# Kernel optimization log

Hardware: AMD Instinct MI355X
Metric: run time of the kernel (lower is better)

The kernel has to match this reference:

```python
import jax, jax.numpy as jnp
import numpy as np

# Block(type='a'): dim=256, mlp_ratio=2, qk_dim=64, att_cr=0.5 (pdim=128), sr=2, inp_group=1
DIM, QK, PD, HID, SR = 256, 64, 128, 512, 2
EPS = 1e-5
SCALE = QK ** -0.5


def _conv(x, w, stride=1, pad=0, groups=1):
    return jax.lax.conv_general_dilated(
        x, w, (stride, stride), [(pad, pad), (pad, pad)],
        feature_group_count=groups,
        dimension_numbers=('NCHW', 'OIHW', 'NCHW'))


def _bn(x, s, b):
    # BatchNorm2d in inference/reparam form: per-channel affine
    return x * s[:, None, None] + b[:, None, None]


def setup_inputs() -> dict:
    key = jax.random.key(0)
    ks = jax.random.split(key, 16)
    B, H, W = 16, 64, 64
    x = jax.random.normal(ks[0], (B, DIM, H, W), jnp.float32)
    def w(k, shape):  # conv weights
        return jax.random.normal(k, shape, jnp.float32) * 0.02
    def sb(k, c):     # bn scale / bias
        k1, k2 = jax.random.split(k)
        return (1.0 + 0.1 * jax.random.normal(k1, (c,), jnp.float32),
                0.1 * jax.random.normal(k2, (c,), jnp.float32))
    s_in, b_in = sb(ks[2], 2 * QK + DIM)
    s_k, b_k = sb(ks[4], QK)
    s_v, b_v = sb(ks[6], PD)
    s_out, b_out = sb(ks[8], DIM)
    s1, b1 = sb(ks[10], HID)
    s2, b2 = sb(ks[12], DIM)
    return dict(
        x=x,
        gn_w=1.0 + 0.1 * jax.random.normal(ks[13], (DIM,), jnp.float32),
        gn_b=0.1 * jax.random.normal(ks[14], (DIM,), jnp.float32),
        w_in=w(ks[1], (2 * QK + DIM, DIM, 3, 3)), s_in=s_in, b_in=b_in,
        w_k=w(ks[3], (QK, 1, SR, SR)), s_k=s_k, b_k=b_k,
        w_v=w(ks[5], (PD, 1, SR, SR)), s_v=s_v, b_v=b_v,
        w_out=w(ks[7], (DIM, DIM, 1, 1)), s_out=s_out, b_out=b_out,
        w1=w(ks[9], (HID, DIM, 1, 1)), s1=s1, b1=b1,
        w2=w(ks[11], (DIM, HID, 1, 1)), s2=s2, b2=b2,
    )


def reference(x, gn_w, gn_b, w_in, s_in, b_in, w_k, s_k, b_k, w_v, s_v, b_v,
              w_out, s_out, b_out, w1, s1, b1, w2, s2, b2):
    B, _, H, W = x.shape
    # --- LRSHA branch ---
    # GroupNorm(1, dim): normalize over (C,H,W) per sample, per-channel affine
    mu = jnp.mean(x, axis=(1, 2, 3), keepdims=True)
    var = jnp.var(x, axis=(1, 2, 3), keepdims=True)
    xn = (x - mu) * jax.lax.rsqrt(var + EPS)
    xn = xn * gn_w[:, None, None] + gn_b[:, None, None]
    t = _bn(_conv(xn, w_in, stride=1, pad=1), s_in, b_in)  # [B, 2*QK+DIM, H, W]
    q, k, v, u = jnp.split(t, [QK, 2 * QK, 2 * QK + PD], axis=1)
    k = _bn(_conv(k, w_k, stride=SR, groups=QK), s_k, b_k)  # [B,QK,H/2,W/2]
    v = _bn(_conv(v, w_v, stride=SR, groups=PD), s_v, b_v)  # [B,PD,H/2,W/2]
    qf = q.reshape(B, QK, H * W)          # [B, QK, N]
    kf = k.reshape(B, QK, -1)             # [B, QK, M]
    vf = v.reshape(B, PD, -1)             # [B, PD, M]
    attn = jax.nn.softmax(jnp.einsum('bcn,bcm->bnm', qf, kf) * SCALE, axis=-1)
    a = jnp.einsum('bpm,bnm->bpn', vf, attn).reshape(B, PD, H, W)
    cat = jnp.concatenate([a, u], axis=1)  # [B, DIM, H, W]
    att_out = _bn(_conv(jax.nn.relu(cat), w_out), s_out, b_out)
    x1 = x + att_out  # residual
    # --- FFN branch (1x1 conv -> ReLU -> 1x1 conv) ---
    h = jax.nn.relu(_bn(_conv(x1, w1), s1, b1))
    ffn = _bn(_conv(h, w2), s2, b2)
    return x1 + ffn
```

## Files before the change

kernel.cpp:

```cpp
#include <hip/hip_runtime.h>
#include <hip/hip_bf16.h>

#define DIM 256
#define QK 64
#define PD 128
#define HID 512
#define NPX 4096
#define NB 16
#define SCALE 0.125f
#define GN_EPS 1e-5f

typedef short bf16x8 __attribute__((ext_vector_type(8)));
typedef float f32x4 __attribute__((ext_vector_type(4)));
#define MFMA16(a, b, c) __builtin_amdgcn_mfma_f32_16x16x32_bf16(a, b, c, 0, 0, 0)

__device__ __forceinline__ unsigned f2b(float f) {
    unsigned u = __float_as_uint(f);
    return (u + 0x7fffu + ((u >> 16) & 1u)) >> 16;
}
__device__ __forceinline__ float b2f(unsigned short s) {
    return __uint_as_float((unsigned)s << 16);
}

__global__ __launch_bounds__(256) void gn_part_kernel(const float* __restrict__ x, float* __restrict__ part) {
    int chunk = blockIdx.x, b = blockIdx.y;
    const float* xp = x + (size_t)b * (DIM * NPX) + (size_t)chunk * 16384;
    float s = 0.f, ss = 0.f;
    for (int i = threadIdx.x; i < 16384; i += 256) { float v = xp[i]; s += v; ss += v * v; }
    for (int off = 32; off > 0; off >>= 1) { s += __shfl_down(s, off); ss += __shfl_down(ss, off); }
    __shared__ float red[8];
    int w = threadIdx.x >> 6;
    if ((threadIdx.x & 63) == 0) { red[w * 2] = s; red[w * 2 + 1] = ss; }
    __syncthreads();
    if (threadIdx.x == 0) {
        float S = red[0] + red[2] + red[4] + red[6];
        float SS = red[1] + red[3] + red[5] + red[7];
        part[(b * 64 + chunk) * 2] = S;
        part[(b * 64 + chunk) * 2 + 1] = SS;
    }
}

__global__ __launch_bounds__(256) void gn_final_kernel(const float* __restrict__ part,
                                                       const float* __restrict__ gn_w, const float* __restrict__ gn_b,
                                                       float* __restrict__ Aarr, float* __restrict__ Barr) {
    int b = blockIdx.x;
    float s = 0.f, ss = 0.f;
    if (threadIdx.x < 64) {
        s = part[(b * 64 + threadIdx.x) * 2];
        ss = part[(b * 64 + threadIdx.x) * 2 + 1];
        for (int off = 32; off > 0; off >>= 1) { s += __shfl_down(s, off); ss += __shfl_down(ss, off); }
    }
    __shared__ float sh[2];
    if (threadIdx.x == 0) {
        const float invN = 1.f / (float)(DIM * NPX);
        float mu = s * invN;
        float var = ss * invN - mu * mu;
        sh[0] = mu; sh[1] = rsqrtf(var + GN_EPS);
    }
    __syncthreads();
    float mu = sh[0], rstd = sh[1];
    int c = threadIdx.x;
    float g = gn_w[c] * rstd;
    Aarr[b * 256 + c] = g;
    Barr[b * 256 + c] = gn_b[c] - mu * g;
}

__global__ __launch_bounds__(256) void xnb_kernel(const float* __restrict__ x,
                                                  const float* __restrict__ Aarr, const float* __restrict__ Barr,
                                                  unsigned short* __restrict__ xb) {
    int y = blockIdx.x, b = blockIdx.y;
    int tid = threadIdx.x;
    __shared__ unsigned short tile[64 * 264];
    const float* xr = x + ((size_t)b << 20) + (size_t)y * 64;
    const float* Ab = Aarr + b * 256;
    const float* Bb = Barr + b * 256;
    for (int it = 0; it < 64; it++) {
        int lin = it * 256 + tid;
        int c = lin >> 6, px = lin & 63;
        float v = fmaf(xr[((size_t)c << 12) + px], Ab[c], Bb[c]);
        tile[px * 264 + c] = (unsigned short)f2b(v);
    }
    __syncthreads();
    unsigned short* ob = xb + (((size_t)(b * 64 + y)) << 14);
    for (int it = 0; it < 8; it++) {
        int lin = it * 256 + tid;
        int px = lin >> 5, g = lin & 31;
        *(uint4*)&ob[px * 256 + g * 8] = *(const uint4*)&tile[px * 264 + g * 8];
    }
}

__global__ __launch_bounds__(256) void wcvt_kernel(const float* __restrict__ w_in, const float* __restrict__ w_out,
                                                   const float* __restrict__ w1, const float* __restrict__ w2,
                                                   unsigned short* __restrict__ wb2, unsigned short* __restrict__ wob,
                                                   unsigned short* __restrict__ w1b, unsigned short* __restrict__ w2b) {
    int idx = blockIdx.x * 256 + threadIdx.x;
    if (idx < 884736) {
        int ci = idx & 31;
        int oc = (idx >> 5) % 384;
        int tapck = idx / 12288;
        int ck = tapck / 9, tap = tapck % 9;
        wb2[idx] = (unsigned short)f2b(w_in[((size_t)oc * 256 + ck * 32 + ci) * 9 + tap]);
    } else if (idx < 950272) {
        int j = idx - 884736;
        wob[j] = (unsigned short)f2b(w_out[j]);
    } else if (idx < 1081344) {
        int j = idx - 950272;
        w1b[j] = (unsigned short)f2b(w1[j]);
    } else if (idx < 1212416) {
        int j = idx - 1081344;
        w2b[j] = (unsigned short)f2b(w2[j]);
    }
}

__global__ __launch_bounds__(256, 3) void conv3_mfma_kernel(const unsigned short* __restrict__ xb,
                                                            const unsigned short* __restrict__ wb2,
                                                            const float* __restrict__ s_in, const float* __restrict__ b_in,
                                                            unsigned short* __restrict__ tcl) {
    int wgid = blockIdx.x;
    int tile = (wgid & 7) * 96 + (wgid >> 3);
    int ocb = tile % 6;
    int tmp = tile / 6;
    int rg2 = tmp & 7, b = tmp >> 3;
    int tid = threadIdx.x;
    int w = tid >> 6, lane = tid & 63, g = lane >> 4, l15 = lane & 15;
    __shared__ unsigned short xs[6 * 66 * 40];
    int oc0 = ocb * 64;
    if (tid < 48) {
        int row = tid >> 3, cp = (tid >> 2) & 1, gg = tid & 3;
        int col = cp ? 65 : 0;
        *(uint4*)&xs[(row * 66 + col) * 40 + gg * 8] = make_uint4(0, 0, 0, 0);
    }
    const unsigned short* xg = xb + ((size_t)b << 20);
    for (int half = 0; half < 2; half++) {
        int y0 = rg2 * 8 + half * 4;
        f32x4 acc[4][4];
#pragma unroll
        for (int o = 0; o < 4; o++)
#pragma unroll
            for (int p = 0; p < 4; p++)
#pragma unroll
                for (int r = 0; r < 4; r++) acc[o][p][r] = 0.f;
        for (int ck = 0; ck < 8; ck++) {
            int ci0 = ck * 32;
            __syncthreads();
#pragma unroll
            for (int it = 0; it < 6; it++) {
                int lin = it * 256 + tid;
                int gg = lin & 3, col = (lin >> 2) & 63, row = lin >> 8;
                int y = y0 - 1 + row;
                uint4 val = make_uint4(0, 0, 0, 0);
                if (y >= 0 && y < 64)
                    val = *(const uint4*)(xg + (((size_t)(y * 64 + col)) << 8) + ci0 + gg * 8);
                *(uint4*)&xs[(row * 66 + col + 1) * 40 + gg * 8] = val;
            }
            __syncthreads();
            const unsigned short* wp = wb2 + (size_t)ck * 9 * 384 * 32;
#pragma unroll
            for (int tap = 0; tap < 9; tap++) {
                int dy = tap / 3, dx = tap % 3;
                bf16x8 Af[4], Bf[4];
#pragma unroll
                for (int o = 0; o < 4; o++)
                    Af[o] = *(const bf16x8*)(wp + ((size_t)tap * 384 + oc0 + o * 16 + l15) * 32 + g * 8);
#pragma unroll
                for (int p = 0; p < 4; p++)
                    Bf[p] = *(const bf16x8*)&xs[((w + dy) * 66 + p * 16 + l15 + dx) * 40 + g * 8];
#pragma unroll
                for (int o = 0; o < 4; o++)
#pragma unroll
                    for (int p = 0; p < 4; p++)
                        acc[o][p] = MFMA16(Af[o], Bf[p], acc[o][p]);
            }
        }
        int y = y0 + w;
        unsigned short* tout = tcl + ((size_t)(b * 4096 + y * 64)) * 384;
#pragma unroll
        for (int o = 0; o < 4; o++) {
            int ocb4 = oc0 + o * 16 + 4 * g;
            float s0 = s_in[ocb4], s1 = s_in[ocb4 + 1], s2 = s_in[ocb4 + 2], s3 = s_in[ocb4 + 3];
            float b0 = b_in[ocb4], b1 = b_in[ocb4 + 1], b2 = b_in[ocb4 + 2], b3 = b_in[ocb4 + 3];
#pragma unroll
            for (int p = 0; p < 4; p++) {
                ushort4 h;
                h.x = (unsigned short)f2b(fmaf(acc[o][p][0], s0, b0));
                h.y = (unsigned short)f2b(fmaf(acc[o][p][1], s1, b1));
                h.z = (unsigned short)f2b(fmaf(acc[o][p][2], s2, b2));
                h.w = (unsigned short)f2b(fmaf(acc[o][p][3], s3, b3));
                *(ushort4*)&tout[(size_t)(p * 16 + l15) * 384 + ocb4] = h;
            }
        }
    }
}

__global__ __launch_bounds__(256) void dw_kernel(const unsigned short* __restrict__ tcl,
                                                 const float* __restrict__ w_k, const float* __restrict__ s_k, const float* __restrict__ b_k,
                                                 const float* __restrict__ w_v, const float* __restrict__ s_v, const float* __restrict__ b_v,
                                                 unsigned short* __restrict__ kd_t, unsigned short* __restrict__ vd_b) {
    int mg = blockIdx.x, b = blockIdx.y;
    int m0 = mg * 64;
    int tid = threadIdx.x;
    __shared__ unsigned short vt[128 * 68];
    {
        int c = tid & 63;
        float4 wk4 = *(const float4*)(w_k + c * 4);
        float sc = s_k[c], bi = b_k[c];
#pragma unroll 4
        for (int it = 0; it < 16; it++) {
            int ml = it * 4 + (tid >> 6);
            int m = m0 + ml, yo = m >> 5, xo = m & 31;
            const unsigned short* s = tcl + ((size_t)(b * 4096 + yo * 128 + xo * 2)) * 384 + 64 + c;
            float v = wk4.x * b2f(s[0]) + wk4.y * b2f(s[384]) + wk4.z * b2f(s[24576]) + wk4.w * b2f(s[24960]);
            kd_t[((size_t)(b * 1024 + m) << 6) + c] = (unsigned short)f2b(fmaf(v, sc, bi));
        }
    }
    {
        int c2 = tid & 127;
        float4 wv4 = *(const float4*)(w_v + c2 * 4);
        float sc = s_v[c2], bi = b_v[c2];
#pragma unroll 4
        for (int it = 0; it < 32; it++) {
            int ml = it * 2 + (tid >> 7);
            int m = m0 + ml, yo = m >> 5, xo = m & 31;
            const unsigned short* s = tcl + ((size_t)(b * 4096 + yo * 128 + xo * 2)) * 384 + 128 + c2;
            float v = wv4.x * b2f(s[0]) + wv4.y * b2f(s[384]) + wv4.z * b2f(s[24576]) + wv4.w * b2f(s[24960]);
            vt[c2 * 68 + ml] = (unsigned short)f2b(fmaf(v, sc, bi));
        }
    }
    __syncthreads();
    {
        int c2 = tid >> 1, part = tid & 1;
        unsigned short* dst = vd_b + (((size_t)(b * 128 + c2)) << 10) + m0 + part * 32;
        const unsigned short* src = &vt[c2 * 68 + part * 32];
#pragma unroll
        for (int j = 0; j < 8; j++)
            *(ushort4*)(dst + j * 4) = *(const ushort4*)(src + j * 4);
    }
}

__global__ __launch_bounds__(256) void attn_mfma_kernel(const unsigned short* __restrict__ tcl,
                                                        const unsigned short* __restrict__ kd_t,
                                                        const unsigned short* __restrict__ vd_b,
                                                        unsigned short* __restrict__ apx) {
    int tid = threadIdx.x;
    int wid = tid >> 6, lane = tid & 63;
    int g = lane >> 4, l15 = lane & 15;
    int b = blockIdx.y;
    int n0 = (blockIdx.x * 4 + wid) * 32;

    __shared__ char KsB[8192];
    __shared__ char VsB[16384];
    __shared__ unsigned short ot[4][32][136];

    bf16x8 qf[2][2];
#pragma unroll
    for (int nf = 0; nf < 2; nf++)
#pragma unroll
        for (int kc = 0; kc < 2; kc++)
            qf[nf][kc] = *(const bf16x8*)(tcl + ((size_t)(b * 4096 + n0 + 16 * nf + l15)) * 384 + kc * 32 + g * 8);

    f32x4 O[8][2];
#pragma unroll
    for (int pt = 0; pt < 8; pt++)
#pragma unroll
        for (int nf = 0; nf < 2; nf++)
#pragma unroll
            for (int r = 0; r < 4; r++) O[pt][nf][r] = 0.f;
    float mr[2] = {-1e30f, -1e30f}, lr[2] = {0.f, 0.f};

    const unsigned short* kb = kd_t + ((size_t)b << 16);
    const unsigned short* vb = vd_b + ((size_t)(b * 128) << 10);

    union BU { unsigned u[4]; bf16x8 v; };
    int srcA = l15 + ((g & 1) << 5);
    int srcB = srcA + 16;
    bool hi = (g >> 1) != 0;
    int srow = tid >> 3, sch = tid & 7;

    for (int mt = 0; mt < 16; mt++) {
        int m0 = mt * 64;
        __syncthreads();
#pragma unroll
        for (int it = 0; it < 2; it++) {
            int row = it * 32 + srow;
            uint4 v = *(const uint4*)(kb + (((size_t)(m0 + row)) << 6) + sch * 8);
            *(uint4*)(KsB + row * 128 + ((sch * 16) ^ ((row & 7) << 4))) = v;
        }
#pragma unroll
        for (int it = 0; it < 4; it++) {
            int row = it * 32 + srow;
            uint4 v = *(const uint4*)(vb + (((size_t)row) << 10) + m0 + sch * 8);
            *(uint4*)(VsB + row * 128 + ((sch * 16) ^ ((row & 7) << 4))) = v;
        }
        __syncthreads();
        f32x4 sp[4][2];
#pragma unroll
        for (int f = 0; f < 4; f++)
#pragma unroll
            for (int nf = 0; nf < 2; nf++)
#pragma unroll
                for (int r = 0; r < 4; r++) sp[f][nf][r] = 0.f;
#pragma unroll
        for (int f = 0; f < 4; f++) {
#pragma unroll
            for (int kc = 0; kc < 2; kc++) {
                bf16x8 kf = *(const bf16x8*)(KsB + (16 * f + l15) * 128 + ((kc * 64 + g * 16) ^ ((l15 & 7) << 4)));
                sp[f][0] = MFMA16(kf, qf[0][kc], sp[f][0]);
                sp[f][1] = MFMA16(kf, qf[1][kc], sp[f][1]);
            }
        }
        BU Bp[2][2];
#pragma unroll
        for (int nf = 0; nf < 2; nf++) {
            float tmax = -1e30f;
#pragma unroll
            for (int f = 0; f < 4; f++)
#pragma unroll
                for (int r = 0; r < 4; r++) tmax = fmaxf(tmax, sp[f][nf][r]);
            tmax = fmaxf(tmax, __shfl_xor(tmax, 16));
            tmax = fmaxf(tmax, __shfl_xor(tmax, 32));
            float newm = fmaxf(mr[nf], tmax * SCALE);
            float fac = __expf(mr[nf] - newm);
            float ps = 0.f;
            unsigned pl[4], ph[4];
#pragma unroll
            for (int f = 0; f < 4; f++) {
                float p0 = __expf(fmaf(sp[f][nf][0], SCALE, -newm));
                float p1 = __expf(fmaf(sp[f][nf][1], SCALE, -newm));
                float p2 = __expf(fmaf(sp[f][nf][2], SCALE, -newm));
                float p3 = __expf(fmaf(sp[f][nf][3], SCALE, -newm));
                ps += (p0 + p1) + (p2 + p3);
                pl[f] = f2b(p0) | (f2b(p1) << 16);
                ph[f] = f2b(p2) | (f2b(p3) << 16);
            }
            ps += __shfl_xor(ps, 16);
            ps += __shfl_xor(ps, 32);
            lr[nf] = fmaf(lr[nf], fac, ps);
            mr[nf] = newm;
#pragma unroll
            for (int pt = 0; pt < 8; pt++)
#pragma unroll
                for (int r = 0; r < 4; r++) O[pt][nf][r] *= fac;
#pragma unroll
            for (int kc = 0; kc < 2; kc++) {
                unsigned a0 = (unsigned)__shfl((int)pl[2 * kc], srcA);
                unsigned a1 = (unsigned)__shfl((int)ph[2 * kc], srcA);
                unsigned b0 = (unsigned)__shfl((int)pl[2 * kc + 1], srcA);
                unsigned b1 = (unsigned)__shfl((int)ph[2 * kc + 1], srcA);
                unsigned a2 = (unsigned)__shfl((int)pl[2 * kc], srcB);
                unsigned a3 = (unsigned)__shfl((int)ph[2 * kc], srcB);
                unsigned b2 = (unsigned)__shfl((int)pl[2 * kc + 1], srcB);
                unsigned b3 = (unsigned)__shfl((int)ph[2 * kc + 1], srcB);
                Bp[nf][kc].u[0] = hi ? b0 : a0;
                Bp[nf][kc].u[1] = hi ? b1 : a1;
                Bp[nf][kc].u[2] = hi ? b2 : a2;
                Bp[nf][kc].u[3] = hi ? b3 : a3;
            }
        }
#pragma unroll
        for (int pt = 0; pt < 8; pt++) {
            int p = pt * 16 + l15;
#pragma unroll
            for (int kc = 0; kc < 2; kc++) {
                bf16x8 vf = *(const bf16x8*)(VsB + p * 128 + ((kc * 64 + g * 16) ^ ((p & 7) << 4)));
                O[pt][0] = MFMA16(vf, Bp[0][kc].v, O[pt][0]);
                O[pt][1] = MFMA16(vf, Bp[1][kc].v, O[pt][1]);
            }
        }
    }
    float inv0 = 1.f / lr[0], inv1 = 1.f / lr[1];
#pragma unroll
    for (int pt = 0; pt < 8; pt++) {
#pragma unroll
        for (int r = 0; r < 4; r++) {
            int prow = pt * 16 + 4 * g + r;
            ot[wid][l15][prow]      = (unsigned short)f2b(fmaxf(O[pt][0][r] * inv0, 0.f));
            ot[wid][l15 + 16][prow] = (unsigned short)f2b(fmaxf(O[pt][1][r] * inv1, 0.f));
        }
    }
#pragma unroll
    for (int j = 0; j < 8; j++) {
        int lin = j * 64 + lane;
        int row = lin >> 4, cg = lin & 15;
        *(uint4*)&apx[((size_t)(b * 4096 + n0 + row)) * 128 + cg * 8] = *(const uint4*)&ot[wid][row][cg * 8];
    }
}

__global__ __launch_bounds__(256) void catconv_mfma_kernel(const unsigned short* __restrict__ apx,
                                                           const unsigned short* __restrict__ tcl,
                                                           const unsigned short* __restrict__ wob,
                                                           const float* __restrict__ x,
                                                           const float* __restrict__ s_out, const float* __restrict__ b_out,
                                                           float* __restrict__ out, unsigned short* __restrict__ x1cl) {
    int tid = threadIdx.x;
    int w = tid >> 6, lane = tid & 63, g = lane >> 4, l15 = lane & 15;
    int b = blockIdx.z;
    int px0 = blockIdx.x * 256 + w * 64;
    int co0 = blockIdx.y * 64;
    f32x4 acc[4][4];
#pragma unroll
    for (int o = 0; o < 4; o++)
#pragma unroll
        for (int p = 0; p < 4; p++)
#pragma unroll
            for (int r = 0; r < 4; r++) acc[o][p][r] = 0.f;
    const unsigned short* ab = apx + (((size_t)b * 4096) << 7);
    const unsigned short* ub = tcl + ((size_t)b * 4096) * 384 + 256;
    for (int kc = 0; kc < 8; kc++) {
        bf16x8 Af[4], Bf[4];
#pragma unroll
        for (int o = 0; o < 4; o++)
            Af[o] = *(const bf16x8*)(wob + (size_t)(co0 + o * 16 + l15) * 256 + kc * 32 + g * 8);
        if (kc < 4) {
#pragma unroll
            for (int p = 0; p < 4; p++)
                Bf[p] = *(const bf16x8*)(ab + ((size_t)(px0 + p * 16 + l15) << 7) + kc * 32 + g * 8);
        } else {
#pragma unroll
            for (int p = 0; p < 4; p++) {
                bf16x8 v = *(const bf16x8*)(ub + (size_t)(px0 + p * 16 + l15) * 384 + (kc - 4) * 32 + g * 8);
#pragma unroll
                for (int j = 0; j < 8; j++) {
                    unsigned short s = (unsigned short)v[j];
                    v[j] = (short)((s & 0x8000u) ? 0 : s);
                }
                Bf[p] = v;
            }
        }
#pragma unroll
        for (int o = 0; o < 4; o++)
#pragma unroll
            for (int p = 0; p < 4; p++)
                acc[o][p] = MFMA16(Af[o], Bf[p], acc[o][p]);
    }
#pragma unroll
    for (int o = 0; o < 4; o++) {
        int co_b = co0 + o * 16 + 4 * g;
#pragma unroll
        for (int r = 0; r < 4; r++) {
            int co = co_b + r;
            float sc = s_out[co], bi = b_out[co];
            size_t base = (((size_t)b * 256 + co) << 12) + px0 + l15;
#pragma unroll
            for (int p = 0; p < 4; p++) {
                float res = x[base + p * 16] + fmaf(acc[o][p][r], sc, bi);
                out[base + p * 16] = res;
                acc[o][p][r] = res;
            }
        }
#pragma unroll
        for (int p = 0; p < 4; p++) {
            ushort4 h;
            h.x = (unsigned short)f2b(acc[o][p][0]);
            h.y = (unsigned short)f2b(acc[o][p][1]);
            h.z = (unsigned short)f2b(acc[o][p][2]);
            h.w = (unsigned short)f2b(acc[o][p][3]);
            *(ushort4*)&x1cl[((size_t)(b * 4096 + px0 + p * 16 + l15)) * 256 + co_b] = h;
        }
    }
}

__global__ __launch_bounds__(256) void ffn1_mfma_kernel(const unsigned short* __restrict__ x1cl,
                                                        const unsigned short* __restrict__ w1b,
                                                        const float* __restrict__ s1, const float* __restrict__ b1,
                                                        unsigned short* __restrict__ hcl) {
    int tid = threadIdx.x;
    int w = tid >> 6, lane = tid & 63, g = lane >> 4, l15 = lane & 15;
    int b = blockIdx.z;
    int px0 = blockIdx.x * 256 + w * 64;
    int hc0 = blockIdx.y * 64;
    f32x4 acc[4][4];
#pragma unroll
    for (int p = 0; p < 4; p++)
#pragma unroll
        for (int o = 0; o < 4; o++)
#pragma unroll
            for (int r = 0; r < 4; r++) acc[p][o][r] = 0.f;
    const unsigned short* xb = x1cl + (((size_t)b * 4096) << 8);
    for (int kc = 0; kc < 8; kc++) {
        bf16x8 Af[4], Bf[4];
#pragma unroll
        for (int p = 0; p < 4; p++)
            Af[p] = *(const bf16x8*)(xb + ((size_t)(px0 + p * 16 + l15) << 8) + kc * 32 + g * 8);
#pragma unroll
        for (int o = 0; o < 4; o++)
            Bf[o] = *(const bf16x8*)(w1b + (size_t)(hc0 + o * 16 + l15) * 256 + kc * 32 + g * 8);
#pragma unroll
        for (int p = 0; p < 4; p++)
#pragma unroll
            for (int o = 0; o < 4; o++)
                acc[p][o] = MFMA16(Af[p], Bf[o], acc[p][o]);
    }
    unsigned short* hb = hcl + (((size_t)b * 4096) << 9);
#pragma unroll
    for (int o = 0; o < 4; o++) {
        int hc = hc0 + o * 16 + l15;
        float sc = s1[hc], bi = b1[hc];
#pragma unroll
        for (int p = 0; p < 4; p++) {
#pragma unroll
            for (int r = 0; r < 4; r++) {
                int px = px0 + p * 16 + 4 * g + r;
                hb[((size_t)px << 9) + hc] = (unsigned short)f2b(fmaxf(fmaf(acc[p][o][r], sc, bi), 0.f));
            }
        }
    }
}

__global__ __launch_bounds__(256) void ffn2_mfma_kernel(const unsigned short* __restrict__ hcl,
                                                        const unsigned short* __restrict__ w2b,
                                                        const float* __restrict__ s2, const float* __restrict__ b2,
                                                        float* __restrict__ out) {
    int tid = threadIdx.x;
    int w = tid >> 6, lane = tid & 63, g = lane >> 4, l15 = lane & 15;
    int b = blockIdx.z;
    int px0 = blockIdx.x * 256 + w * 64;
    int co0 = blockIdx.y * 64;
    f32x4 acc[4][4];
#pragma unroll
    for (int o = 0; o < 4; o++)
#pragma unroll
        for (int p = 0; p < 4; p++)
#pragma unroll
            for (int r = 0; r < 4; r++) acc[o][p][r] = 0.f;
    const unsigned short* hb = hcl + (((size_t)b * 4096) << 9);
    for (int kc = 0; kc < 16; kc++) {
        bf16x8 Af[4], Bf[4];
#pragma unroll
        for (int o = 0; o < 4; o++)
            Af[o] = *(const bf16x8*)(w2b + (size_t)(co0 + o * 16 + l15) * 512 + kc * 32 + g * 8);
#pragma unroll
        for (int p = 0; p < 4; p++)
            Bf[p] = *(const bf16x8*)(hb + ((size_t)(px0 + p * 16 + l15) << 9) + kc * 32 + g * 8);
#pragma unroll
        for (int o = 0; o < 4; o++)
#pragma unroll
            for (int p = 0; p < 4; p++)
                acc[o][p] = MFMA16(Af[o], Bf[p], acc[o][p]);
    }
#pragma unroll
    for (int o = 0; o < 4; o++) {
#pragma unroll
        for (int r = 0; r < 4; r++) {
            int co = co0 + o * 16 + 4 * g + r;
            float sc = s2[co], bi = b2[co];
            size_t base = (((size_t)b * 256 + co) << 12) + px0 + l15;
#pragma unroll
            for (int p = 0; p < 4; p++)
                out[base + p * 16] = out[base + p * 16] + fmaf(acc[o][p][r], sc, bi);
        }
    }
}

extern "C" void kernel_launch(void* const* d_in, const int* in_sizes, int n_in,
                              void* d_out, int out_size, void* d_ws, size_t ws_size,
                              hipStream_t stream) {
    const float* x    = (const float*)d_in[0];
    const float* gn_w = (const float*)d_in[1];
    const float* gn_b = (const float*)d_in[2];
    const float* w_in = (const float*)d_in[3];
    const float* s_in = (const float*)d_in[4];
    const float* b_in = (const float*)d_in[5];
    const float* w_k  = (const float*)d_in[6];
    const float* s_k  = (const float*)d_in[7];
    const float* b_k  = (const float*)d_in[8];
    const float* w_v  = (const float*)d_in[9];
    const float* s_v  = (const float*)d_in[10];
    const float* b_v  = (const float*)d_in[11];
    const float* w_out= (const float*)d_in[12];
    const float* s_out= (const float*)d_in[13];
    const float* b_out= (const float*)d_in[14];
    const float* w1   = (const float*)d_in[15];
    const float* s1   = (const float*)d_in[16];
    const float* b1   = (const float*)d_in[17];
    const float* w2   = (const float*)d_in[18];
    const float* s2   = (const float*)d_in[19];
    const float* b2   = (const float*)d_in[20];
    float* out = (float*)d_out;
    float* ws = (float*)d_ws;

    float* part = ws;
    float* Aarr = ws + 2048;
    float* Barr = ws + 6144;
    unsigned short* tcl = (unsigned short*)(ws + 10240);
    unsigned short* xb   = (unsigned short*)(ws + 12593152);
    unsigned short* x1cl = (unsigned short*)(ws + 12593152);
    unsigned short* apx  = (unsigned short*)(ws + 20981760);
    unsigned short* hcl  = (unsigned short*)(ws + 20981760);
    unsigned short* kd_t = (unsigned short*)(ws + 37758976);
    unsigned short* vd_b = (unsigned short*)(ws + 38283264);
    unsigned short* wb2  = (unsigned short*)(ws + 39331840);
    unsigned short* wob  = (unsigned short*)(ws + 39774208);
    unsigned short* w1b  = (unsigned short*)(ws + 39806976);
    unsigned short* w2b  = (unsigned short*)(ws + 39872512);

    gn_part_kernel<<<dim3(64, 16), 256, 0, stream>>>(x, part);
    gn_final_kernel<<<16, 256, 0, stream>>>(part, gn_w, gn_b, Aarr, Barr);
    xnb_kernel<<<dim3(64, 16), 256, 0, stream>>>(x, Aarr, Barr, xb);
    wcvt_kernel<<<4736, 256, 0, stream>>>(w_in, w_out, w1, w2, wb2, wob, w1b, w2b);
    conv3_mfma_kernel<<<768, 256, 0, stream>>>(xb, wb2, s_in, b_in, tcl);
    dw_kernel<<<dim3(16, 16), 256, 0, stream>>>(tcl, w_k, s_k, b_k, w_v, s_v, b_v, kd_t, vd_b);
    attn_mfma_kernel<<<dim3(32, 16), 256, 0, stream>>>(tcl, kd_t, vd_b, apx);
    catconv_mfma_kernel<<<dim3(16, 4, 16), 256, 0, stream>>>(apx, tcl, wob, x, s_out, b_out, out, x1cl);
    ffn1_mfma_kernel<<<dim3(16, 8, 16), 256, 0, stream>>>(x1cl, w1b, s1, b1, hcl);
    ffn2_mfma_kernel<<<dim3(16, 4, 16), 256, 0, stream>>>(hcl, w2b, s2, b2, out);
}
```

Baseline: 516.2 us.

## Halve attention rows per wave, add lazy softmax rescale, prefetch conv3 weights

The attention kernel now handles 16 query rows per wave instead of 32, doubling the grid and adding a launch-bounds occupancy hint. Shared memory shrinks by reusing the K/V buffers for the output transpose. Softmax switches to exp2 with a prescaled constant and skips rescaling O unless the running max grows by more than a threshold. Separately, the 3x3 conv kernel double-buffers weight fragments across taps behind a sched_barrier. The trade-off is that K/V tiles are reloaded by twice as many blocks, and the lazy rescale lets unnormalised values grow before the final division.

```diff
diff --git a/kernel.cpp b/kernel.cpp
--- a/kernel.cpp
+++ b/kernel.cpp
@@ -155,21 +155,32 @@
             }
             __syncthreads();
             const unsigned short* wp = wb2 + (size_t)ck * 9 * 384 * 32;
+            bf16x8 AfC[4], AfN[4];
+#pragma unroll
+            for (int o = 0; o < 4; o++)
+                AfC[o] = *(const bf16x8*)(wp + ((size_t)0 * 384 + oc0 + o * 16 + l15) * 32 + g * 8);
 #pragma unroll
             for (int tap = 0; tap < 9; tap++) {
                 int dy = tap / 3, dx = tap % 3;
-                bf16x8 Af[4], Bf[4];
-#pragma unroll
-                for (int o = 0; o < 4; o++)
-                    Af[o] = *(const bf16x8*)(wp + ((size_t)tap * 384 + oc0 + o * 16 + l15) * 32 + g * 8);
+                if (tap < 8) {
+#pragma unroll
+                    for (int o = 0; o < 4; o++)
+                        AfN[o] = *(const bf16x8*)(wp + ((size_t)(tap + 1) * 384 + oc0 + o * 16 + l15) * 32 + g * 8);
+                }
+                bf16x8 Bf[4];
 #pragma unroll
                 for (int p = 0; p < 4; p++)
                     Bf[p] = *(const bf16x8*)&xs[((w + dy) * 66 + p * 16 + l15 + dx) * 40 + g * 8];
+                __builtin_amdgcn_sched_barrier(0);
 #pragma unroll
                 for (int o = 0; o < 4; o++)
 #pragma unroll
                     for (int p = 0; p < 4; p++)
-                        acc[o][p] = MFMA16(Af[o], Bf[p], acc[o][p]);
+                        acc[o][p] = MFMA16(AfC[o], Bf[p], acc[o][p]);
+                if (tap < 8) {
+#pragma unroll
+                    for (int o = 0; o < 4; o++) AfC[o] = AfN[o];
+                }
             }
         }
         int y = y0 + w;
@@ -237,35 +248,33 @@
     }
 }
 
-__global__ __launch_bounds__(256) void attn_mfma_kernel(const unsigned short* __restrict__ tcl,
-                                                        const unsigned short* __restrict__ kd_t,
-                                                        const unsigned short* __restrict__ vd_b,
-                                                        unsigned short* __restrict__ apx) {
+__global__ __launch_bounds__(256, 4) void attn_mfma_kernel(const unsigned short* __restrict__ tcl,
+                                                           const unsigned short* __restrict__ kd_t,
+                                                           const unsigned short* __restrict__ vd_b,
+                                                           unsigned short* __restrict__ apx) {
     int tid = threadIdx.x;
     int wid = tid >> 6, lane = tid & 63;
     int g = lane >> 4, l15 = lane & 15;
     int b = blockIdx.y;
-    int n0 = (blockIdx.x * 4 + wid) * 32;
-
-    __shared__ char KsB[8192];
-    __shared__ char VsB[16384];
-    __shared__ unsigned short ot[4][32][136];
-
-    bf16x8 qf[2][2];
-#pragma unroll
-    for (int nf = 0; nf < 2; nf++)
-#pragma unroll
-        for (int kc = 0; kc < 2; kc++)
-            qf[nf][kc] = *(const bf16x8*)(tcl + ((size_t)(b * 4096 + n0 + 16 * nf + l15)) * 384 + kc * 32 + g * 8);
-
-    f32x4 O[8][2];
+    int n0 = (blockIdx.x * 4 + wid) * 16;
+
+    __shared__ char smem[24576];
+    char* KsB = smem;
+    char* VsB = smem + 8192;
+
+    const float SC2 = 0.18033688011112042f;
+
+    bf16x8 qf[2];
+#pragma unroll
+    for (int kc = 0; kc < 2; kc++)
+        qf[kc] = *(const bf16x8*)(tcl + ((size_t)(b * 4096 + n0 + l15)) * 384 + kc * 32 + g * 8);
+
+    f32x4 O[8];
 #pragma unroll
     for (int pt = 0; pt < 8; pt++)
 #pragma unroll
-        for (int nf = 0; nf < 2; nf++)
-#pragma unroll
-            for (int r = 0; r < 4; r++) O[pt][nf][r] = 0.f;
-    float mr[2] = {-1e30f, -1e30f}, lr[2] = {0.f, 0.f};
+        for (int r = 0; r < 4; r++) O[pt][r] = 0.f;
+    float mr = -1e30f, lr = 0.f;
 
     const unsigned short* kb = kd_t + ((size_t)b << 16);
     const unsigned short* vb = vd_b + ((size_t)(b * 128) << 10);
@@ -274,87 +283,85 @@
     int srcA = l15 + ((g & 1) << 5);
     int srcB = srcA + 16;
     bool hi = (g >> 1) != 0;
-    int srow = tid >> 3, sch = tid & 7;
+    int srow8 = tid >> 3, sch8 = tid & 7;
 
     for (int mt = 0; mt < 16; mt++) {
         int m0 = mt * 64;
         __syncthreads();
 #pragma unroll
         for (int it = 0; it < 2; it++) {
-            int row = it * 32 + srow;
-            uint4 v = *(const uint4*)(kb + (((size_t)(m0 + row)) << 6) + sch * 8);
-            *(uint4*)(KsB + row * 128 + ((sch * 16) ^ ((row & 7) << 4))) = v;
+            int row = it * 32 + srow8;
+            uint4 v = *(const uint4*)(kb + (((size_t)(m0 + row)) << 6) + sch8 * 8);
+            *(uint4*)(KsB + row * 128 + ((sch8 * 16) ^ ((row & 7) << 4))) = v;
         }
 #pragma unroll
         for (int it = 0; it < 4; it++) {
-            int row = it * 32 + srow;
-            uint4 v = *(const uint4*)(vb + (((size_t)row) << 10) + m0 + sch * 8);
-            *(uint4*)(VsB + row * 128 + ((sch * 16) ^ ((row & 7) << 4))) = v;
+            int row = it * 32 + srow8;
+            uint4 v = *(const uint4*)(vb + (((size_t)row) << 10) + m0 + sch8 * 8);
+            *(uint4*)(VsB + row * 128 + ((sch8 * 16) ^ ((row & 7) << 4))) = v;
         }
         __syncthreads();
-        f32x4 sp[4][2];
+        f32x4 sp[4];
 #pragma unroll
         for (int f = 0; f < 4; f++)
 #pragma unroll
-            for (int nf = 0; nf < 2; nf++)
-#pragma unroll
-                for (int r = 0; r < 4; r++) sp[f][nf][r] = 0.f;
+            for (int r = 0; r < 4; r++) sp[f][r] = 0.f;
 #pragma unroll
         for (int f = 0; f < 4; f++) {
 #pragma unroll
             for (int kc = 0; kc < 2; kc++) {
                 bf16x8 kf = *(const bf16x8*)(KsB + (16 * f + l15) * 128 + ((kc * 64 + g * 16) ^ ((l15 & 7) << 4)));
-                sp[f][0] = MFMA16(kf, qf[0][kc], sp[f][0]);
-                sp[f][1] = MFMA16(kf, qf[1][kc], sp[f][1]);
-            }
-        }
-        BU Bp[2][2];
-#pragma unroll
-        for (int nf = 0; nf < 2; nf++) {
-            float tmax = -1e30f;
-#pragma unroll
-            for (int f = 0; f < 4; f++)
-#pragma unroll
-                for (int r = 0; r < 4; r++) tmax = fmaxf(tmax, sp[f][nf][r]);
-            tmax = fmaxf(tmax, __shfl_xor(tmax, 16));
-            tmax = fmaxf(tmax, __shfl_xor(tmax, 32));
-            float newm = fmaxf(mr[nf], tmax * SCALE);
-            float fac = __expf(mr[nf] - newm);
-            float ps = 0.f;
-            unsigned pl[4], ph[4];
-#pragma unroll
-            for (int f = 0; f < 4; f++) {
-                float p0 = __expf(fmaf(sp[f][nf][0], SCALE, -newm));
-                float p1 = __expf(fmaf(sp[f][nf][1], SCALE, -newm));
-                float p2 = __expf(fmaf(sp[f][nf][2], SCALE, -newm));
-                float p3 = __expf(fmaf(sp[f][nf][3], SCALE, -newm));
-                ps += (p0 + p1) + (p2 + p3);
-                pl[f] = f2b(p0) | (f2b(p1) << 16);
-                ph[f] = f2b(p2) | (f2b(p3) << 16);
-            }
-            ps += __shfl_xor(ps, 16);
-            ps += __shfl_xor(ps, 32);
-            lr[nf] = fmaf(lr[nf], fac, ps);
-            mr[nf] = newm;
+                sp[f] = MFMA16(kf, qf[kc], sp[f]);
+            }
+        }
+        float tmax = -1e30f;
+#pragma unroll
+        for (int f = 0; f < 4; f++)
+#pragma unroll
+            for (int r = 0; r < 4; r++) tmax = fmaxf(tmax, sp[f][r]);
+        tmax = fmaxf(tmax, __shfl_xor(tmax, 16));
+        tmax = fmaxf(tmax, __shfl_xor(tmax, 32));
+        float tm2 = tmax * SC2;
+        if (!__all(tm2 <= mr + 11.0f)) {
+            float newm = fmaxf(mr, tm2);
+            float fac = exp2f(mr - newm);
+            lr *= fac;
 #pragma unroll
             for (int pt = 0; pt < 8; pt++)
 #pragma unroll
-                for (int r = 0; r < 4; r++) O[pt][nf][r] *= fac;
-#pragma unroll
-            for (int kc = 0; kc < 2; kc++) {
-                unsigned a0 = (unsigned)__shfl((int)pl[2 * kc], srcA);
-                unsigned a1 = (unsigned)__shfl((int)ph[2 * kc], srcA);
-                unsigned b0 = (unsigned)__shfl((int)pl[2 * kc + 1], srcA);
-                unsigned b1 = (unsigned)__shfl((int)ph[2 * kc + 1], srcA);
-                unsigned a2 = (unsigned)__shfl((int)pl[2 * kc], srcB);
-                unsigned a3 = (unsigned)__shfl((int)ph[2 * kc], srcB);
-                unsigned b2 = (unsigned)__shfl((int)pl[2 * kc + 1], srcB);
-                unsigned b3 = (unsigned)__shfl((int)ph[2 * kc + 1], srcB);
-                Bp[nf][kc].u[0] = hi ? b0 : a0;
-                Bp[nf][kc].u[1] = hi ? b1 : a1;
-                Bp[nf][kc].u[2] = hi ? b2 : a2;
-                Bp[nf][kc].u[3] = hi ? b3 : a3;
-            }
+                for (int r = 0; r < 4; r++) O[pt][r] *= fac;
+            mr = newm;
+        }
+        float ps = 0.f;
+        unsigned pl[4], ph[4];
+#pragma unroll
+        for (int f = 0; f < 4; f++) {
+            float p0 = exp2f(fmaf(sp[f][0], SC2, -mr));
+            float p1 = exp2f(fmaf(sp[f][1], SC2, -mr));
+            float p2 = exp2f(fmaf(sp[f][2], SC2, -mr));
+            float p3 = exp2f(fmaf(sp[f][3], SC2, -mr));
+            ps += (p0 + p1) + (p2 + p3);
+            pl[f] = f2b(p0) | (f2b(p1) << 16);
+            ph[f] = f2b(p2) | (f2b(p3) << 16);
+        }
+        ps += __shfl_xor(ps, 16);
+        ps += __shfl_xor(ps, 32);
+        lr += ps;
+        BU Bp[2];
+#pragma unroll
+        for (int kc = 0; kc < 2; kc++) {
+            unsigned a0 = (unsigned)__shfl((int)pl[2 * kc], srcA);
+            unsigned a1 = (unsigned)__shfl((int)ph[2 * kc], srcA);
+            unsigned b0 = (unsigned)__shfl((int)pl[2 * kc + 1], srcA);
+            unsigned b1 = (unsigned)__shfl((int)ph[2 * kc + 1], srcA);
+            unsigned a2 = (unsigned)__shfl((int)pl[2 * kc], srcB);
+            unsigned a3 = (unsigned)__shfl((int)ph[2 * kc], srcB);
+            unsigned b2 = (unsigned)__shfl((int)pl[2 * kc + 1], srcB);
+            unsigned b3 = (unsigned)__shfl((int)ph[2 * kc + 1], srcB);
+            Bp[kc].u[0] = hi ? b0 : a0;
+            Bp[kc].u[1] = hi ? b1 : a1;
+            Bp[kc].u[2] = hi ? b2 : a2;
+            Bp[kc].u[3] = hi ? b3 : a3;
         }
 #pragma unroll
         for (int pt = 0; pt < 8; pt++) {
@@ -362,23 +369,23 @@
 #pragma unroll
             for (int kc = 0; kc < 2; kc++) {
                 bf16x8 vf = *(const bf16x8*)(VsB + p * 128 + ((kc * 64 + g * 16) ^ ((p & 7) << 4)));
-                O[pt][0] = MFMA16(vf, Bp[0][kc].v, O[pt][0]);
-                O[pt][1] = MFMA16(vf, Bp[1][kc].v, O[pt][1]);
-            }
-        }
-    }
-    float inv0 = 1.f / lr[0], inv1 = 1.f / lr[1];
+                O[pt] = MFMA16(vf, Bp[kc].v, O[pt]);
+            }
+        }
+    }
+    __syncthreads();
+    unsigned short (*ot)[16][136] = (unsigned short (*)[16][136])smem;
+    float inv = 1.f / lr;
 #pragma unroll
     for (int pt = 0; pt < 8; pt++) {
 #pragma unroll
         for (int r = 0; r < 4; r++) {
             int prow = pt * 16 + 4 * g + r;
-            ot[wid][l15][prow]      = (unsigned short)f2b(fmaxf(O[pt][0][r] * inv0, 0.f));
-            ot[wid][l15 + 16][prow] = (unsigned short)f2b(fmaxf(O[pt][1][r] * inv1, 0.f));
-        }
-    }
-#pragma unroll
-    for (int j = 0; j < 8; j++) {
+            ot[wid][l15][prow] = (unsigned short)f2b(fmaxf(O[pt][r] * inv, 0.f));
+        }
+    }
+#pragma unroll
+    for (int j = 0; j < 4; j++) {
         int lin = j * 64 + lane;
         int row = lin >> 4, cg = lin & 15;
         *(uint4*)&apx[((size_t)(b * 4096 + n0 + row)) * 128 + cg * 8] = *(const uint4*)&ot[wid][row][cg * 8];
@@ -599,7 +606,7 @@
     wcvt_kernel<<<4736, 256, 0, stream>>>(w_in, w_out, w1, w2, wb2, wob, w1b, w2b);
     conv3_mfma_kernel<<<768, 256, 0, stream>>>(xb, wb2, s_in, b_in, tcl);
     dw_kernel<<<dim3(16, 16), 256, 0, stream>>>(tcl, w_k, s_k, b_k, w_v, s_v, b_v, kd_t, vd_b);
-    attn_mfma_kernel<<<dim3(32, 16), 256, 0, stream>>>(tcl, kd_t, vd_b, apx);
+    attn_mfma_kernel<<<dim3(64, 16), 256, 0, stream>>>(tcl, kd_t, vd_b, apx);
     catconv_mfma_kernel<<<dim3(16, 4, 16), 256, 0, stream>>>(apx, tcl, wob, x, s_out, b_out, out, x1cl);
     ffn1_mfma_kernel<<<dim3(16, 8, 16), 256, 0, stream>>>(x1cl, w1b, s1, b1, hcl);
     ffn2_mfma_kernel<<<dim3(16, 4, 16), 256, 0, stream>>>(hcl, w2b, s2, b2, out);
```

After: 468.2 us, median of 2. -9.3%, faster.
